# Performance work log

Measured on AMD Instinct MI355X. Metric: run time of the kernel, lower is better.

## Reference

```python
import jax, jax.numpy as jnp
import numpy as np

EOS = 1e-10
ALPHA = 0.5
TEMPERATURE = 1.0
BIAS = 0.0001
N_NODES = 8192
N_EDGES = 262144
INPUT_DIM = 512
HIDDEN = 128


def setup_inputs() -> dict:
    key = jax.random.key(0)
    ks = jax.random.split(key, 7)
    features = jax.random.normal(ks[0], (N_NODES, INPUT_DIM), dtype=jnp.float32)
    W_emb = jax.random.normal(ks[1], (HIDDEN, INPUT_DIM), dtype=jnp.float32) * (1.0 / np.sqrt(INPUT_DIM))
    b_emb = jax.random.normal(ks[2], (HIDDEN,), dtype=jnp.float32) * 0.01
    W_edge = jax.random.normal(ks[3], (1, 2 * HIDDEN), dtype=jnp.float32) * (1.0 / np.sqrt(2 * HIDDEN))
    b_edge = jax.random.normal(ks[4], (1,), dtype=jnp.float32) * 0.01
    noise = jax.random.uniform(ks[5], (N_EDGES,), dtype=jnp.float32)
    edges = jax.random.randint(ks[6], (2, N_EDGES), 0, N_NODES, dtype=jnp.int64 if jax.config.jax_enable_x64 else jnp.int32)
    return {"features": features, "W_emb": W_emb, "b_emb": b_emb,
            "W_edge": W_edge, "b_edge": b_edge, "noise": noise, "edges": edges}


def _sym_normalize(adj):
    # inv_sqrt_degree[:,None] * adj * inv_sqrt_degree[None,:]
    inv_sqrt_deg = 1.0 / (jnp.sqrt(adj.sum(axis=1)) + EOS)
    return adj * inv_sqrt_deg[:, None] * inv_sqrt_deg[None, :]


def reference(features, W_emb, b_emb, W_edge, b_edge, noise, edges):
    n = N_NODES
    # node embedding: single Linear + ReLU
    h = jax.nn.relu(features @ W_emb.T + b_emb)            # [N, H]
    e0, e1 = edges[0], edges[1]
    h0, h1 = h[e0], h[e1]                                   # [E, H] gathers
    Wa, Wb = W_edge[0, :HIDDEN], W_edge[0, HIDDEN:]
    s1 = h0 @ Wa + h1 @ Wb + b_edge[0]                       # edge_mlp(cat(h0,h1))
    s2 = h1 @ Wa + h0 @ Wb + b_edge[0]                       # edge_mlp(cat(h1,h0))
    raw = 0.5 * (s1 + s2)                                    # [E]
    # gumbel gate: eps = (bias-(1-bias))*rand + (1-bias)
    eps = (BIAS - (1.0 - BIAS)) * noise + (1.0 - BIAS)
    gate = (jnp.log(eps) - jnp.log1p(-eps) + raw) / TEMPERATURE
    weights_lp = jax.nn.sigmoid(gate)                        # [E]
    weights_hp = 1.0 - weights_lp
    eye = jnp.eye(n, dtype=features.dtype)
    # scatter edge weights to dense adjacency (assignment semantics, like torch adj[e0,e1]=w)
    adj_lp = jnp.zeros((n, n), dtype=features.dtype).at[e0, e1].set(weights_lp) + eye
    adj_lp = _sym_normalize(adj_lp)
    adj_hp = jnp.zeros((n, n), dtype=features.dtype).at[e0, e1].set(weights_hp) + eye
    adj_hp = _sym_normalize(adj_hp)
    mask = jnp.zeros((n, n), dtype=features.dtype).at[e0, e1].set(1.0)
    adj_hp = eye - adj_hp * mask * ALPHA
    return (adj_lp, adj_hp, weights_lp, weights_hp)
```

## Files before the change

### kernel.cpp

```cpp
#include <hip/hip_runtime.h>
#include <cstdint>
#include <cstddef>

#define N_NODES 8192
#define N_EDGES 262144
#define INPUT_DIM 512
#define HIDDEN 128
#define ALPHA 0.5f
#define EOS 1e-10f
#define BCAP 128
#define LDA 40

typedef float v4 __attribute__((ext_vector_type(4)));
typedef __attribute__((ext_vector_type(8))) short short8;
typedef __attribute__((ext_vector_type(4))) float floatx4;

__device__ inline unsigned short f2bf(float x) {
    unsigned u = __builtin_bit_cast(unsigned, x);
    return (unsigned short)((u + 0x7FFFu + ((u >> 16) & 1u)) >> 16);
}
__device__ inline unsigned pack2(float a, float b) {
    return (unsigned)f2bf(a) | ((unsigned)f2bf(b) << 16);
}

__global__ __launch_bounds__(256) void k1_g(
    const float* __restrict__ F, const float* __restrict__ W,
    const float* __restrict__ bemb, const float* __restrict__ Wedge,
    float* __restrict__ g, int* __restrict__ cnt)
{
    __shared__ unsigned short As[32 * LDA];
    __shared__ unsigned short Bs[128 * LDA];
    __shared__ float part[4][16];
    int tid = threadIdx.x;
    int gt = blockIdx.x * 256 + tid;
    if (gt < N_NODES) cnt[gt] = 0;

    int node0 = blockIdx.x * 32;
    int lane = tid & 63, wave = tid >> 6;
    int ml = lane & 15, q = lane >> 4;
    int strip = wave & 1, hq = wave >> 1;

    int arow = tid >> 3, ac4 = (tid & 7) * 4;
    const float* Fp = &F[(size_t)(node0 + arow) * INPUT_DIM + ac4];
    const float* Wp = &W[(size_t)arow * INPUT_DIM + ac4];

    float4 aR = *(const float4*)Fp;
    float4 bR0 = *(const float4*)(Wp + (size_t)(0 * 32) * INPUT_DIM);
    float4 bR1 = *(const float4*)(Wp + (size_t)(1 * 32) * INPUT_DIM);
    float4 bR2 = *(const float4*)(Wp + (size_t)(2 * 32) * INPUT_DIM);
    float4 bR3 = *(const float4*)(Wp + (size_t)(3 * 32) * INPUT_DIM);

    floatx4 acc[4];
#pragma unroll
    for (int j = 0; j < 4; j++) acc[j] = 0.f;

    for (int s = 0; s < 16; s++) {
        { uint2 p; p.x = pack2(aR.x, aR.y); p.y = pack2(aR.z, aR.w);
          *(uint2*)&As[arow * LDA + ac4] = p; }
        { uint2 p; p.x = pack2(bR0.x, bR0.y); p.y = pack2(bR0.z, bR0.w);
          *(uint2*)&Bs[(0 * 32 + arow) * LDA + ac4] = p; }
        { uint2 p; p.x = pack2(bR1.x, bR1.y); p.y = pack2(bR1.z, bR1.w);
          *(uint2*)&Bs[(1 * 32 + arow) * LDA + ac4] = p; }
        { uint2 p; p.x = pack2(bR2.x, bR2.y); p.y = pack2(bR2.z, bR2.w);
          *(uint2*)&Bs[(2 * 32 + arow) * LDA + ac4] = p; }
        { uint2 p; p.x = pack2(bR3.x, bR3.y); p.y = pack2(bR3.z, bR3.w);
          *(uint2*)&Bs[(3 * 32 + arow) * LDA + ac4] = p; }
        __syncthreads();
        if (s < 15) {
            int off = (s + 1) * 32;
            aR  = *(const float4*)(Fp + off);
            bR0 = *(const float4*)(Wp + off + (size_t)(0 * 32) * INPUT_DIM);
            bR1 = *(const float4*)(Wp + off + (size_t)(1 * 32) * INPUT_DIM);
            bR2 = *(const float4*)(Wp + off + (size_t)(2 * 32) * INPUT_DIM);
            bR3 = *(const float4*)(Wp + off + (size_t)(3 * 32) * INPUT_DIM);
        }
        short8 a = *(const short8*)&As[(strip * 16 + ml) * LDA + q * 8];
#pragma unroll
        for (int j = 0; j < 4; j++) {
            short8 b = *(const short8*)&Bs[((hq * 4 + j) * 16 + ml) * LDA + q * 8];
            acc[j] = __builtin_amdgcn_mfma_f32_16x16x32_bf16(a, b, acc[j], 0, 0, 0);
        }
        __syncthreads();
    }
    float sr[4] = {0.f, 0.f, 0.f, 0.f};
#pragma unroll
    for (int j = 0; j < 4; j++) {
        int hcol = (hq * 4 + j) * 16 + ml;
        float u = Wedge[hcol] + Wedge[HIDDEN + hcol];
        float bb = bemb[hcol];
#pragma unroll
        for (int rg = 0; rg < 4; rg++) {
            float h = acc[j][rg] + bb;
            sr[rg] += (h > 0.f ? h : 0.f) * u;
        }
    }
#pragma unroll
    for (int m = 1; m < 16; m <<= 1) {
#pragma unroll
        for (int rg = 0; rg < 4; rg++) sr[rg] += __shfl_xor(sr[rg], m, 16);
    }
    if (ml == 0) {
#pragma unroll
        for (int rg = 0; rg < 4; rg++) part[wave][q * 4 + rg] = sr[rg];
    }
    __syncthreads();
    if (tid < 32) {
        int st = tid >> 4, ni = tid & 15;
        g[node0 + st * 16 + ni] = part[st][ni] + part[st + 2][ni];
    }
}

__global__ __launch_bounds__(256) void k_edge(
    const int* __restrict__ edges, const float* __restrict__ noise,
    const float* __restrict__ g, const float* __restrict__ bedge,
    float* __restrict__ wlp, float* __restrict__ whp,
    int* __restrict__ cnt, int* __restrict__ bucket)
{
    int i = blockIdx.x * 256 + threadIdx.x;
    int e0 = edges[i], e1 = edges[N_EDGES + i];
    float raw = 0.5f * (g[e0] + g[e1]) + bedge[0];
    float eps = -0.9998f * noise[i] + 0.9999f;
    float gate = logf(eps) - log1pf(-eps) + raw;
    float w = 1.f / (1.f + expf(-gate));
    wlp[i] = w;
    whp[i] = 1.f - w;
    int pos = atomicAdd(&cnt[e0], 1);
    if (pos < BCAP) bucket[e0 * BCAP + pos] = i;
}

__global__ __launch_bounds__(256) void k_deginv(
    const int* __restrict__ edges, const float* __restrict__ wlp,
    const float* __restrict__ whp, const int* __restrict__ cnt,
    int* __restrict__ bucket, float* __restrict__ bval_lp, float* __restrict__ bval_hp,
    float* __restrict__ inv_lp, float* __restrict__ inv_hp)
{
    __shared__ int cols[2][BCAP];
    __shared__ int eidx[2][BCAP];
    __shared__ float plp[4], php[4];
    int tid = threadIdx.x;
    int half = tid >> 7, lt = tid & 127;
    int r = blockIdx.x * 2 + half;
    int d = cnt[r]; if (d > BCAP) d = BCAP;
    int i = -1, c = -1;
    if (lt < d) {
        i = bucket[r * BCAP + lt];
        c = edges[N_EDGES + i];
        cols[half][lt] = c;
        eidx[half][lt] = i;
    }
    __syncthreads();
    float sl = 0.f, sh = 0.f;
    if (lt < d) {
        bool win = true;
        for (int j = 0; j < d; j++)
            if (cols[half][j] == c && eidx[half][j] > i) { win = false; break; }
        if (win) {
            sl = wlp[i]; sh = whp[i];
            bucket[r * BCAP + lt] = c;
            bval_lp[r * BCAP + lt] = sl;
            bval_hp[r * BCAP + lt] = sh;
        } else {
            bucket[r * BCAP + lt] = -1;
        }
    }
#pragma unroll
    for (int m = 1; m < 64; m <<= 1) {
        sl += __shfl_xor(sl, m, 64);
        sh += __shfl_xor(sh, m, 64);
    }
    int wv = tid >> 6;
    if ((tid & 63) == 0) { plp[wv] = sl; php[wv] = sh; }
    __syncthreads();
    if (lt == 0) {
        float l = plp[half * 2] + plp[half * 2 + 1];
        float h = php[half * 2] + php[half * 2 + 1];
        inv_lp[r] = 1.f / (sqrtf(l + 1.f) + EOS);
        inv_hp[r] = 1.f / (sqrtf(h + 1.f) + EOS);
    }
}

__global__ __launch_bounds__(256) void k_fill(
    const int* __restrict__ cnt, const int* __restrict__ bucket,
    const float* __restrict__ bval_lp, const float* __restrict__ bval_hp,
    const float* __restrict__ inv_lp, const float* __restrict__ inv_hp,
    float* __restrict__ LP, float* __restrict__ HP)
{
    __shared__ unsigned bm[256];
    __shared__ int   s_col[BCAP + 1];
    __shared__ float s_vlp[BCAP + 1];
    __shared__ float s_vhp[BCAP + 1];
    __shared__ int   s_d;
    int r = blockIdx.x, tid = threadIdx.x;
    bm[tid] = 0;
    int d = cnt[r]; if (d > BCAP) d = BCAP;
    float irl = inv_lp[r], irh = inv_hp[r];
    __syncthreads();
    int c = -1;
    if (tid < d) c = bucket[r * BCAP + tid];
    if (tid < d) s_col[tid] = c;
    if (c >= 0) {
        float w_lp = bval_lp[r * BCAP + tid];
        float w_hp = bval_hp[r * BCAP + tid];
        float icl = inv_lp[c], ich = inv_hp[c];
        float diag = (c == r) ? 1.f : 0.f;
        s_vlp[tid] = (w_lp + diag) * irl * icl;
        s_vhp[tid] = diag - (w_hp + diag) * irh * ich * ALPHA;
        atomicOr(&bm[c >> 5], 1u << (c & 31));
    }
    __syncthreads();
    if (tid == 0) {
        int dd = d;
        if (!((bm[r >> 5] >> (r & 31)) & 1u)) {
            s_col[dd] = r; s_vlp[dd] = irl * irl; s_vhp[dd] = 1.0f;
            bm[r >> 5] |= 1u << (r & 31);
            dd++;
        }
        s_d = dd;
    }
    __syncthreads();
    int dd = s_d;
    float* LPr = LP + (size_t)r * N_NODES;
    float* HPr = HP + (size_t)r * N_NODES;
#pragma unroll
    for (int i = 0; i < 8; i++) {
        int ch = i * 256 + tid;
        unsigned nib = (bm[ch >> 3] >> ((ch & 7) * 4)) & 0xFu;
        v4 lp = 0.f, hp = 0.f;
        if (nib) {
            for (int e = 0; e < dd; e++) {
                int cc = s_col[e];
                if ((cc >> 2) == ch) {
                    int sl = cc & 3;
                    ((float*)&lp)[sl] = s_vlp[e];
                    ((float*)&hp)[sl] = s_vhp[e];
                }
            }
        }
        __builtin_nontemporal_store(lp, (v4*)&LPr[ch * 4]);
        __builtin_nontemporal_store(hp, (v4*)&HPr[ch * 4]);
    }
}

extern "C" void kernel_launch(void* const* d_in, const int* in_sizes, int n_in,
                              void* d_out, int out_size, void* d_ws, size_t ws_size,
                              hipStream_t stream) {
    const float* F     = (const float*)d_in[0];
    const float* W     = (const float*)d_in[1];
    const float* bemb  = (const float*)d_in[2];
    const float* Wedge = (const float*)d_in[3];
    const float* bedge = (const float*)d_in[4];
    const float* noise = (const float*)d_in[5];
    const int*   edges = (const int*)d_in[6];

    const size_t N2 = (size_t)N_NODES * N_NODES;
    float* out = (float*)d_out;
    float* LP  = out;
    float* HP  = out + N2;
    float* wlp = HP + N2;
    float* whp = wlp + N_EDGES;

    char* ws = (char*)d_ws;
    float* g       = (float*)(ws);
    int*   cnt     = (int*)  (ws + 32768);
    float* inv_lp  = (float*)(ws + 65536);
    float* inv_hp  = (float*)(ws + 98304);
    int*   bucket  = (int*)  (ws + 131072);
    float* bval_lp = (float*)(ws + 131072 + (size_t)N_NODES * BCAP * 4);
    float* bval_hp = (float*)(ws + 131072 + 2 * (size_t)N_NODES * BCAP * 4);

    k1_g<<<256, 256, 0, stream>>>(F, W, bemb, Wedge, g, cnt);
    k_edge<<<N_EDGES / 256, 256, 0, stream>>>(edges, noise, g, bedge,
                                              wlp, whp, cnt, bucket);
    k_deginv<<<N_NODES / 2, 256, 0, stream>>>(edges, wlp, whp, cnt, bucket,
                                              bval_lp, bval_hp, inv_lp, inv_hp);
    k_fill<<<N_NODES, 256, 0, stream>>>(cnt, bucket, bval_lp, bval_hp,
                                        inv_lp, inv_hp, LP, HP);
}
```

Before: 614.9 us.

## Pre-convert GEMM inputs to bf16 and pack edge col/weight into bucket entries

Adds a conversion kernel that writes bf16 copies of features and W, and rewrites the embedding GEMM to load MFMA fragments straight from global memory with no LDS staging or barriers. Edge buckets now hold packed (column, edge index) plus the weight as int2, so the dedup and fill kernels no longer gather edges, wlp and whp or use separate value arrays. This trades an extra kernel launch and an extra pass over the features for less scattered traffic in the bucket stages. The total is likely dominated by the 512MB dense output writes, which this change does not touch.

```diff
diff --git a/kernel.cpp b/kernel.cpp
--- a/kernel.cpp
+++ b/kernel.cpp
@@ -9,7 +9,6 @@
 #define ALPHA 0.5f
 #define EOS 1e-10f
 #define BCAP 128
-#define LDA 40
 
 typedef float v4 __attribute__((ext_vector_type(4)));
 typedef __attribute__((ext_vector_type(8))) short short8;
@@ -19,102 +18,87 @@
     unsigned u = __builtin_bit_cast(unsigned, x);
     return (unsigned short)((u + 0x7FFFu + ((u >> 16) & 1u)) >> 16);
 }
-__device__ inline unsigned pack2(float a, float b) {
-    return (unsigned)f2bf(a) | ((unsigned)f2bf(b) << 16);
+
+__global__ __launch_bounds__(256) void k0_conv(
+    const float* __restrict__ F, const float* __restrict__ W,
+    unsigned short* __restrict__ F16, unsigned short* __restrict__ W16,
+    int* __restrict__ cnt)
+{
+    int t = blockIdx.x * 256 + threadIdx.x;
+    if (t < N_NODES) cnt[t] = 0;
+    {
+        float4 v = *(const float4*)&F[(size_t)t * 4];
+        uint2 p;
+        p.x = (unsigned)f2bf(v.x) | ((unsigned)f2bf(v.y) << 16);
+        p.y = (unsigned)f2bf(v.z) | ((unsigned)f2bf(v.w) << 16);
+        *(uint2*)&F16[(size_t)t * 4] = p;
+    }
+    if (t < 16384) {
+        float4 v = *(const float4*)&W[(size_t)t * 4];
+        uint2 p;
+        p.x = (unsigned)f2bf(v.x) | ((unsigned)f2bf(v.y) << 16);
+        p.y = (unsigned)f2bf(v.z) | ((unsigned)f2bf(v.w) << 16);
+        *(uint2*)&W16[(size_t)t * 4] = p;
+    }
 }
 
 __global__ __launch_bounds__(256) void k1_g(
-    const float* __restrict__ F, const float* __restrict__ W,
+    const unsigned short* __restrict__ F16, const unsigned short* __restrict__ W16,
     const float* __restrict__ bemb, const float* __restrict__ Wedge,
-    float* __restrict__ g, int* __restrict__ cnt)
-{
-    __shared__ unsigned short As[32 * LDA];
-    __shared__ unsigned short Bs[128 * LDA];
+    float* __restrict__ g)
+{
     __shared__ float part[4][16];
     int tid = threadIdx.x;
-    int gt = blockIdx.x * 256 + tid;
-    if (gt < N_NODES) cnt[gt] = 0;
-
-    int node0 = blockIdx.x * 32;
     int lane = tid & 63, wave = tid >> 6;
     int ml = lane & 15, q = lane >> 4;
-    int strip = wave & 1, hq = wave >> 1;
-
-    int arow = tid >> 3, ac4 = (tid & 7) * 4;
-    const float* Fp = &F[(size_t)(node0 + arow) * INPUT_DIM + ac4];
-    const float* Wp = &W[(size_t)arow * INPUT_DIM + ac4];
-
-    float4 aR = *(const float4*)Fp;
-    float4 bR0 = *(const float4*)(Wp + (size_t)(0 * 32) * INPUT_DIM);
-    float4 bR1 = *(const float4*)(Wp + (size_t)(1 * 32) * INPUT_DIM);
-    float4 bR2 = *(const float4*)(Wp + (size_t)(2 * 32) * INPUT_DIM);
-    float4 bR3 = *(const float4*)(Wp + (size_t)(3 * 32) * INPUT_DIM);
-
-    floatx4 acc[4];
-#pragma unroll
-    for (int j = 0; j < 4; j++) acc[j] = 0.f;
-
+    int node0 = blockIdx.x * 16;
+    int h0 = wave * 32;
+
+    const unsigned short* Ap  = &F16[(size_t)(node0 + ml) * INPUT_DIM + q * 8];
+    const unsigned short* Bp0 = &W16[(size_t)(h0 + ml) * INPUT_DIM + q * 8];
+    const unsigned short* Bp1 = &W16[(size_t)(h0 + 16 + ml) * INPUT_DIM + q * 8];
+
+    floatx4 acc0 = 0.f, acc1 = 0.f;
+#pragma unroll 4
     for (int s = 0; s < 16; s++) {
-        { uint2 p; p.x = pack2(aR.x, aR.y); p.y = pack2(aR.z, aR.w);
-          *(uint2*)&As[arow * LDA + ac4] = p; }
-        { uint2 p; p.x = pack2(bR0.x, bR0.y); p.y = pack2(bR0.z, bR0.w);
-          *(uint2*)&Bs[(0 * 32 + arow) * LDA + ac4] = p; }
-        { uint2 p; p.x = pack2(bR1.x, bR1.y); p.y = pack2(bR1.z, bR1.w);
-          *(uint2*)&Bs[(1 * 32 + arow) * LDA + ac4] = p; }
-        { uint2 p; p.x = pack2(bR2.x, bR2.y); p.y = pack2(bR2.z, bR2.w);
-          *(uint2*)&Bs[(2 * 32 + arow) * LDA + ac4] = p; }
-        { uint2 p; p.x = pack2(bR3.x, bR3.y); p.y = pack2(bR3.z, bR3.w);
-          *(uint2*)&Bs[(3 * 32 + arow) * LDA + ac4] = p; }
-        __syncthreads();
-        if (s < 15) {
-            int off = (s + 1) * 32;
-            aR  = *(const float4*)(Fp + off);
-            bR0 = *(const float4*)(Wp + off + (size_t)(0 * 32) * INPUT_DIM);
-            bR1 = *(const float4*)(Wp + off + (size_t)(1 * 32) * INPUT_DIM);
-            bR2 = *(const float4*)(Wp + off + (size_t)(2 * 32) * INPUT_DIM);
-            bR3 = *(const float4*)(Wp + off + (size_t)(3 * 32) * INPUT_DIM);
-        }
-        short8 a = *(const short8*)&As[(strip * 16 + ml) * LDA + q * 8];
-#pragma unroll
-        for (int j = 0; j < 4; j++) {
-            short8 b = *(const short8*)&Bs[((hq * 4 + j) * 16 + ml) * LDA + q * 8];
-            acc[j] = __builtin_amdgcn_mfma_f32_16x16x32_bf16(a, b, acc[j], 0, 0, 0);
-        }
-        __syncthreads();
+        short8 a  = *(const short8*)(Ap  + s * 32);
+        short8 b0 = *(const short8*)(Bp0 + s * 32);
+        short8 b1 = *(const short8*)(Bp1 + s * 32);
+        acc0 = __builtin_amdgcn_mfma_f32_16x16x32_bf16(a, b0, acc0, 0, 0, 0);
+        acc1 = __builtin_amdgcn_mfma_f32_16x16x32_bf16(a, b1, acc1, 0, 0, 0);
     }
     float sr[4] = {0.f, 0.f, 0.f, 0.f};
 #pragma unroll
-    for (int j = 0; j < 4; j++) {
-        int hcol = (hq * 4 + j) * 16 + ml;
-        float u = Wedge[hcol] + Wedge[HIDDEN + hcol];
-        float bb = bemb[hcol];
+    for (int t = 0; t < 2; t++) {
+        int h = h0 + t * 16 + ml;
+        float uu = Wedge[h] + Wedge[HIDDEN + h];
+        float bb = bemb[h];
+        floatx4 ac = t ? acc1 : acc0;
 #pragma unroll
         for (int rg = 0; rg < 4; rg++) {
-            float h = acc[j][rg] + bb;
-            sr[rg] += (h > 0.f ? h : 0.f) * u;
+            float hv = ac[rg] + bb;
+            sr[rg] += (hv > 0.f ? hv : 0.f) * uu;
         }
     }
 #pragma unroll
     for (int m = 1; m < 16; m <<= 1) {
 #pragma unroll
-        for (int rg = 0; rg < 4; rg++) sr[rg] += __shfl_xor(sr[rg], m, 16);
+        for (int rg = 0; rg < 4; rg++) sr[rg] += __shfl_xor(sr[rg], m, 64);
     }
     if (ml == 0) {
 #pragma unroll
         for (int rg = 0; rg < 4; rg++) part[wave][q * 4 + rg] = sr[rg];
     }
     __syncthreads();
-    if (tid < 32) {
-        int st = tid >> 4, ni = tid & 15;
-        g[node0 + st * 16 + ni] = part[st][ni] + part[st + 2][ni];
-    }
+    if (tid < 16)
+        g[node0 + tid] = part[0][tid] + part[1][tid] + part[2][tid] + part[3][tid];
 }
 
 __global__ __launch_bounds__(256) void k_edge(
     const int* __restrict__ edges, const float* __restrict__ noise,
     const float* __restrict__ g, const float* __restrict__ bedge,
     float* __restrict__ wlp, float* __restrict__ whp,
-    int* __restrict__ cnt, int* __restrict__ bucket)
+    int* __restrict__ cnt, int2* __restrict__ buck)
 {
     int i = blockIdx.x * 256 + threadIdx.x;
     int e0 = edges[i], e1 = edges[N_EDGES + i];
@@ -125,43 +109,46 @@
     wlp[i] = w;
     whp[i] = 1.f - w;
     int pos = atomicAdd(&cnt[e0], 1);
-    if (pos < BCAP) bucket[e0 * BCAP + pos] = i;
+    if (pos < BCAP) {
+        int2 pw;
+        pw.x = (e1 << 18) | i;
+        pw.y = __builtin_bit_cast(int, w);
+        buck[e0 * BCAP + pos] = pw;
+    }
 }
 
 __global__ __launch_bounds__(256) void k_deginv(
-    const int* __restrict__ edges, const float* __restrict__ wlp,
-    const float* __restrict__ whp, const int* __restrict__ cnt,
-    int* __restrict__ bucket, float* __restrict__ bval_lp, float* __restrict__ bval_hp,
+    const int* __restrict__ cnt, int2* __restrict__ buck,
     float* __restrict__ inv_lp, float* __restrict__ inv_hp)
 {
-    __shared__ int cols[2][BCAP];
-    __shared__ int eidx[2][BCAP];
+    __shared__ int s_pv[2][BCAP];
     __shared__ float plp[4], php[4];
     int tid = threadIdx.x;
     int half = tid >> 7, lt = tid & 127;
     int r = blockIdx.x * 2 + half;
     int d = cnt[r]; if (d > BCAP) d = BCAP;
-    int i = -1, c = -1;
+    int2 pw; pw.x = -1; pw.y = 0;
     if (lt < d) {
-        i = bucket[r * BCAP + lt];
-        c = edges[N_EDGES + i];
-        cols[half][lt] = c;
-        eidx[half][lt] = i;
+        pw = buck[r * BCAP + lt];
+        s_pv[half][lt] = pw.x;
     }
     __syncthreads();
     float sl = 0.f, sh = 0.f;
     if (lt < d) {
+        int pv = pw.x, c = pv >> 18;
         bool win = true;
-        for (int j = 0; j < d; j++)
-            if (cols[half][j] == c && eidx[half][j] > i) { win = false; break; }
+        for (int j = 0; j < d; j++) {
+            int o = s_pv[half][j];
+            if ((o >> 18) == c && o > pv) { win = false; break; }
+        }
         if (win) {
-            sl = wlp[i]; sh = whp[i];
-            bucket[r * BCAP + lt] = c;
-            bval_lp[r * BCAP + lt] = sl;
-            bval_hp[r * BCAP + lt] = sh;
+            float w = __builtin_bit_cast(float, pw.y);
+            sl = w; sh = 1.f - w;
+            pw.x = c;
         } else {
-            bucket[r * BCAP + lt] = -1;
-        }
+            pw.x = -1;
+        }
+        buck[r * BCAP + lt] = pw;
     }
 #pragma unroll
     for (int m = 1; m < 64; m <<= 1) {
@@ -180,8 +167,7 @@
 }
 
 __global__ __launch_bounds__(256) void k_fill(
-    const int* __restrict__ cnt, const int* __restrict__ bucket,
-    const float* __restrict__ bval_lp, const float* __restrict__ bval_hp,
+    const int* __restrict__ cnt, const int2* __restrict__ buck,
     const float* __restrict__ inv_lp, const float* __restrict__ inv_hp,
     float* __restrict__ LP, float* __restrict__ HP)
 {
@@ -196,16 +182,18 @@
     float irl = inv_lp[r], irh = inv_hp[r];
     __syncthreads();
     int c = -1;
-    if (tid < d) c = bucket[r * BCAP + tid];
-    if (tid < d) s_col[tid] = c;
-    if (c >= 0) {
-        float w_lp = bval_lp[r * BCAP + tid];
-        float w_hp = bval_hp[r * BCAP + tid];
-        float icl = inv_lp[c], ich = inv_hp[c];
-        float diag = (c == r) ? 1.f : 0.f;
-        s_vlp[tid] = (w_lp + diag) * irl * icl;
-        s_vhp[tid] = diag - (w_hp + diag) * irh * ich * ALPHA;
-        atomicOr(&bm[c >> 5], 1u << (c & 31));
+    if (tid < d) {
+        int2 pw = buck[r * BCAP + tid];
+        c = pw.x;
+        s_col[tid] = c;
+        if (c >= 0) {
+            float w = __builtin_bit_cast(float, pw.y);
+            float icl = inv_lp[c], ich = inv_hp[c];
+            float diag = (c == r) ? 1.f : 0.f;
+            s_vlp[tid] = (w + diag) * irl * icl;
+            s_vhp[tid] = diag - ((1.f - w) + diag) * irh * ich * ALPHA;
+            atomicOr(&bm[c >> 5], 1u << (c & 31));
+        }
     }
     __syncthreads();
     if (tid == 0) {
@@ -229,7 +217,7 @@
         if (nib) {
             for (int e = 0; e < dd; e++) {
                 int cc = s_col[e];
-                if ((cc >> 2) == ch) {
+                if (cc >= 0 && (cc >> 2) == ch) {
                     int sl = cc & 3;
                     ((float*)&lp)[sl] = s_vlp[e];
                     ((float*)&hp)[sl] = s_vhp[e];
@@ -260,19 +248,18 @@
     float* whp = wlp + N_EDGES;
 
     char* ws = (char*)d_ws;
-    float* g       = (float*)(ws);
-    int*   cnt     = (int*)  (ws + 32768);
-    float* inv_lp  = (float*)(ws + 65536);
-    float* inv_hp  = (float*)(ws + 98304);
-    int*   bucket  = (int*)  (ws + 131072);
-    float* bval_lp = (float*)(ws + 131072 + (size_t)N_NODES * BCAP * 4);
-    float* bval_hp = (float*)(ws + 131072 + 2 * (size_t)N_NODES * BCAP * 4);
-
-    k1_g<<<256, 256, 0, stream>>>(F, W, bemb, Wedge, g, cnt);
+    float* g      = (float*)(ws);
+    int*   cnt    = (int*)  (ws + 32768);
+    float* inv_lp = (float*)(ws + 65536);
+    float* inv_hp = (float*)(ws + 98304);
+    int2*  buck   = (int2*) (ws + 131072);
+    unsigned short* F16 = (unsigned short*)(ws + 131072 + (size_t)N_NODES * BCAP * 8);
+    unsigned short* W16 = F16 + (size_t)N_NODES * INPUT_DIM;
+
+    k0_conv<<<4096, 256, 0, stream>>>(F, W, F16, W16, cnt);
+    k1_g<<<512, 256, 0, stream>>>(F16, W16, bemb, Wedge, g);
     k_edge<<<N_EDGES / 256, 256, 0, stream>>>(edges, noise, g, bedge,
-                                              wlp, whp, cnt, bucket);
-    k_deginv<<<N_NODES / 2, 256, 0, stream>>>(edges, wlp, whp, cnt, bucket,
-                                              bval_lp, bval_hp, inv_lp, inv_hp);
-    k_fill<<<N_NODES, 256, 0, stream>>>(cnt, bucket, bval_lp, bval_hp,
-                                        inv_lp, inv_hp, LP, HP);
-}
+                                              wlp, whp, cnt, buck);
+    k_deginv<<<N_NODES / 2, 256, 0, stream>>>(cnt, buck, inv_lp, inv_hp);
+    k_fill<<<N_NODES, 256, 0, stream>>>(cnt, buck, inv_lp, inv_hp, LP, HP);
+}
```

Result: no change. 610.1 us (-0.8%).
